# Optimization experiments

Measured on AMD Instinct MI355X. Metric: run time of the kernel, lower is better.

The kernel has to match this reference:

```python
import jax, jax.numpy as jnp
import numpy as np

B, S, D, V = 2, 4096, 2048, 32000
H, HD = 16, 128          # heads, head dim (H*HD == D)
BS = 16                  # block_size
N_ANCH = 128             # num_anchors (static: loss_mask=ones guarantees enough valid positions)
MASK_ID = 31999
DFF = 8192


def rms(x, w, eps=1e-6):
    return x * jax.lax.rsqrt(jnp.mean(x * x, axis=-1, keepdims=True) + eps) * w


def rope(x, pos):
    # x: (..., L, H, hd), pos: (..., L)
    hd = x.shape[-1]
    inv = 1.0 / (10000.0 ** (jnp.arange(0, hd, 2, dtype=jnp.float32) / hd))
    ang = pos[..., None, None].astype(jnp.float32) * inv  # (..., L, 1, hd/2)
    cos, sin = jnp.cos(ang), jnp.sin(ang)
    x1, x2 = x[..., : hd // 2], x[..., hd // 2 :]
    return jnp.concatenate([x1 * cos - x2 * sin, x2 * cos + x1 * sin], axis=-1).astype(x.dtype)


def setup_inputs() -> dict:
    key = jax.random.key(0)
    ks = jax.random.split(key, 12)
    s = 0.02
    return {
        "input_ids": jax.random.randint(ks[0], (B, S), 0, V, dtype=jnp.int32),
        "hidden_states": jax.random.normal(ks[1], (B, S, D), dtype=jnp.float32),
        "loss_mask": jnp.ones((B, S), dtype=jnp.float32),
        "rand_vals": jax.random.uniform(ks[2], (B, S - BS + 1), dtype=jnp.float32),
        "embed_table": jax.random.normal(ks[3], (V, D), dtype=jnp.float32) * s,
        "lm_head_w": jax.random.normal(ks[4], (V, D), dtype=jnp.float32) * s,
        "wq": jax.random.normal(ks[5], (D, D), dtype=jnp.float32) * s,
        "wk": jax.random.normal(ks[6], (D, D), dtype=jnp.float32) * s,
        "wv": jax.random.normal(ks[7], (D, D), dtype=jnp.float32) * s,
        "wo": jax.random.normal(ks[8], (D, D), dtype=jnp.float32) * s,
        "w_gate": jax.random.normal(ks[9], (D, DFF), dtype=jnp.float32) * s,
        "w_up": jax.random.normal(ks[10], (D, DFF), dtype=jnp.float32) * s,
        "w_down": jax.random.normal(ks[11], (DFF, D), dtype=jnp.float32) * s,
        "norm_attn": jnp.ones((D,), dtype=jnp.float32),
        "norm_mlp": jnp.ones((D,), dtype=jnp.float32),
        "norm_out": jnp.ones((D,), dtype=jnp.float32),
        "norm_chs": jnp.ones((D,), dtype=jnp.float32),
    }


def reference(input_ids, hidden_states, loss_mask, rand_vals, embed_table, lm_head_w,
              wq, wk, wv, wo, w_gate, w_up, w_down, norm_attn, norm_mlp, norm_out, norm_chs):
    max_anchor = S - BS
    # ---- anchor sampling: random permutation of valid positions via argsort of rand ----
    valid = loss_mask[:, : max_anchor + 1] > 0.5                       # (B, max_anchor+1)
    valid_counts = valid.sum(axis=1)
    idx = jnp.arange(max_anchor + 1, dtype=jnp.int32)
    masked_idx = jnp.where(valid, idx[None, :], S + 1)
    rv = jnp.where(valid, rand_vals, 2.0)
    order = jnp.argsort(rv, axis=1)
    gathered = jnp.take_along_axis(masked_idx, order, axis=1)
    anchors = jnp.sort(gathered[:, :N_ANCH], axis=1)                   # (B, N)
    keep = jnp.arange(N_ANCH)[None, :] < jnp.minimum(valid_counts, N_ANCH)[:, None]
    anchors = jnp.where(keep, anchors, 0)
    # ---- noise embedding: anchor token at block start, mask token elsewhere ----
    anchor_tok = jnp.take_along_axis(input_ids, jnp.clip(anchors, 0, S - 1), axis=1)
    first_tok = jnp.where(keep, anchor_tok, MASK_ID)
    noise_ids = jnp.full((B, N_ANCH, BS), MASK_ID, dtype=jnp.int32).at[:, :, 0].set(first_tok)
    x = embed_table[noise_ids]                                         # (B,N,BS,D)
    # ---- CHS context hidden: target hidden at anchor-1 ----
    ctx_pos = jnp.maximum(anchors - 1, 0)
    ctx = jnp.take_along_axis(hidden_states, ctx_pos[:, :, None], axis=1)  # (B,N,D)
    # ---- block-diagonal attention: per-block kv = [CHS_i | draft block i] (kv_len=1+BS) ----
    pos_q = anchors[:, :, None] + jnp.arange(BS)[None, None, :]        # (B,N,BS)
    pos_kv = jnp.concatenate([ctx_pos[:, :, None], pos_q], axis=2)     # (B,N,1+BS)
    hq = rms(x, norm_attn)
    hc = rms(ctx, norm_chs)[:, :, None, :]
    kv_in = jnp.concatenate([hc, hq], axis=2)                          # (B,N,1+BS,D)
    q = rope((hq @ wq).reshape(B, N_ANCH, BS, H, HD), pos_q)
    k = rope((kv_in @ wk).reshape(B, N_ANCH, 1 + BS, H, HD), pos_kv)
    v = (kv_in @ wv).reshape(B, N_ANCH, 1 + BS, H, HD)
    scores = jnp.einsum('bnqhd,bnkhd->bnhqk', q, k) * (1.0 / HD ** 0.5)
    attn = jax.nn.softmax(scores, axis=-1)
    out = jnp.einsum('bnhqk,bnkhd->bnqhd', attn, v).reshape(B, N_ANCH, BS, D) @ wo
    out = out * keep[:, :, None, None].astype(out.dtype)               # invalid blocks fully masked
    x = x + out
    h = rms(x, norm_mlp)
    x = x + (jax.nn.silu(h @ w_gate) * (h @ w_up)) @ w_down
    h_out = rms(x, norm_out)
    logits = h_out @ lm_head_w.T                                       # (B,N,BS,V)
    # ---- block-wise CE loss ----
    label_idx = anchors[:, :, None] + jnp.arange(BS)[None, None, :]
    valid_label = label_idx < S
    safe = jnp.minimum(label_idx, S - 1)
    targets = jnp.take_along_axis(jnp.broadcast_to(input_ids[:, None, :], (B, N_ANCH, S)), safe, axis=2)
    lm_g = jnp.take_along_axis(jnp.broadcast_to(loss_mask[:, None, :], (B, N_ANCH, S)), safe, axis=2)
    weight = (keep[:, :, None] & valid_label).astype(jnp.float32)
    weight = weight * (jnp.arange(BS) > 0)[None, None, :].astype(jnp.float32) * lm_g
    logp = jax.nn.log_softmax(logits, axis=-1)
    tok_logp = jnp.take_along_axis(logp, targets[..., None].astype(jnp.int32), axis=-1)[..., 0]
    loss = -(tok_logp * weight).sum() / (weight.sum() + 1e-6)
    pred = jnp.argmax(logits, axis=-1)
    accuracy = ((pred == targets) & (weight > 0.5)).sum().astype(jnp.float32) / (weight.sum() + 1e-6)
    return loss, accuracy
```

## Files before the change

### kernel.cpp

```cpp
#include <hip/hip_runtime.h>
#include <math.h>

typedef unsigned short u16;
typedef unsigned char u8;
typedef short v8s __attribute__((ext_vector_type(8)));
typedef u16   v4u __attribute__((ext_vector_type(4)));
typedef float v4f __attribute__((ext_vector_type(4)));
typedef int   v2i __attribute__((ext_vector_type(2)));

#define DEVFN static __device__ __forceinline__

constexpr int cB = 2, cS = 4096, cD = 2048, cV = 32000, cH = 16, cHD = 128;
constexpr int cBS = 16, cNA = 128, cMASK = 31999, cDFF = 8192;
constexpr int NCAND = cS - cBS + 1;
constexpr int MTOK  = cB * cNA * cBS;
constexpr int MKV   = cB * cNA * 17;
constexpr int NCH   = cV / 128;
constexpr int NCH2  = cV / 256;

constexpr int EPI_BF16 = 0, EPI_SILU = 1, EPI_OEMB = 2, EPI_DOWNACC = 3, EPI_STATS = 4;
constexpr int ASRC_BF16 = 0, ASRC_RMS = 1, ASRC_AOMAP = 2;

struct RmsSrc {
  const float* hs; const float* emb; const float* nattn; const float* nchs;
  const float* rowinv; const int* ftok; const int* cpos;
};

DEVFN u16 f2bf(float f) {
  union { float f; unsigned u; } a; a.f = f;
  unsigned u = a.u;
  u = u + 0x7fffu + ((u >> 16) & 1u);
  return (u16)(u >> 16);
}
DEVFN float bf2f(u16 h) {
  union { unsigned u; float f; } a; a.u = ((unsigned)h) << 16;
  return a.f;
}
DEVFN float waveSum(float v) {
  #pragma unroll
  for (int o = 32; o >= 1; o >>= 1) v += __shfl_xor(v, o);
  return v;
}
DEVFN void gload16(void* lds, const void* g) {
  __builtin_amdgcn_global_load_lds(
      (const __attribute__((address_space(1))) unsigned*)g,
      (__attribute__((address_space(3))) unsigned*)lds, 16, 0, 0);
}
DEVFN int pack4fp8(float a, float b, float c, float d) {
  int p = __builtin_amdgcn_cvt_pk_fp8_f32(a, b, 0, 0);
  p = __builtin_amdgcn_cvt_pk_fp8_f32(c, d, p, 1);
  return p;
}

__global__ void k_select(const float* __restrict__ lmask, const float* __restrict__ rv_in,
                         int* __restrict__ self) {
  int b = blockIdx.x >> 4, chunk = blockIdx.x & 15;
  __shared__ float rvs[4096];
  for (int i = threadIdx.x; i < NCAND; i += 256) {
    bool valid = lmask[(size_t)b * cS + i] > 0.5f;
    rvs[i] = valid ? rv_in[(size_t)b * NCAND + i] : 2.0f;
  }
  __syncthreads();
  int i = chunk * 256 + threadIdx.x;
  if (i < NCAND) {
    float v = rvs[i];
    int rank = 0;
    for (int j = 0; j < NCAND; ++j) {
      float u = rvs[j];
      rank += (u < v) || (u == v && j < i);
    }
    self[(size_t)b * NCAND + i] = (rank < cNA) ? 1 : 0;
  }
}

__global__ void k_anchors(const float* __restrict__ lmask, const int* __restrict__ self,
                          const int* __restrict__ ids, int* __restrict__ anchors,
                          int* __restrict__ keepA, int* __restrict__ ftok, int* __restrict__ cpos) {
  int b = blockIdx.x;
  __shared__ int flags[4096];
  __shared__ int ssum[256];
  __shared__ int soff[257];
  __shared__ int abuf[cNA];
  for (int i = threadIdx.x; i < 4096; i += 256)
    flags[i] = (i < NCAND) ? (self[(size_t)b * NCAND + i] && (lmask[(size_t)b * cS + i] > 0.5f)) : 0;
  if (threadIdx.x < cNA) abuf[threadIdx.x] = 0;
  __syncthreads();
  int s = 0;
  #pragma unroll
  for (int j = 0; j < 16; ++j) s += flags[threadIdx.x * 16 + j];
  ssum[threadIdx.x] = s;
  __syncthreads();
  if (threadIdx.x == 0) {
    int a = 0;
    for (int t = 0; t < 256; ++t) { soff[t] = a; a += ssum[t]; }
    soff[256] = a;
  }
  __syncthreads();
  int nsel = soff[256];
  int p = soff[threadIdx.x];
  for (int j = 0; j < 16; ++j) {
    int i = threadIdx.x * 16 + j;
    if (flags[i]) { if (p < cNA) abuf[p] = i; ++p; }
  }
  __syncthreads();
  if (threadIdx.x < cNA) {
    int q = threadIdx.x;
    int kp = (q < nsel) ? 1 : 0;
    int a = kp ? abuf[q] : 0;
    anchors[b * cNA + q] = a;
    keepA[b * cNA + q] = kp;
    int av = a; if (av < 0) av = 0; if (av > cS - 1) av = cS - 1;
    int tok = ids[(size_t)b * cS + av];
    ftok[b * cNA + q] = kp ? tok : cMASK;
    cpos[b * cNA + q] = (a - 1 > 0) ? (a - 1) : 0;
  }
}

__global__ void k_rowinv(const float* __restrict__ hs, const float* __restrict__ emb,
                         const int* __restrict__ ftok, const int* __restrict__ cpos,
                         float* __restrict__ rowinv) {
  int r = blockIdx.x;
  int j = r % 17, bn = r / 17, b = bn >> 7;
  const float* src = (j == 0) ? hs + ((size_t)b * cS + cpos[bn]) * cD
                              : emb + (size_t)((j == 1) ? ftok[bn] : cMASK) * cD;
  float ss = 0.f;
  for (int d = threadIdx.x; d < cD; d += 256) { float v = src[d]; ss += v * v; }
  ss = waveSum(ss);
  __shared__ float red[4];
  if ((threadIdx.x & 63) == 0) red[threadIdx.x >> 6] = ss;
  __syncthreads();
  if (threadIdx.x == 0) {
    float tot = red[0] + red[1] + red[2] + red[3];
    rowinv[r] = 1.0f / sqrtf(tot / cD + 1e-6f);
  }
}

__global__ void k_build2(const float* __restrict__ hs, const float* __restrict__ emb,
                         const float* __restrict__ nattn, const float* __restrict__ nchs,
                         const int* __restrict__ ftok, const int* __restrict__ cpos,
                         u16* __restrict__ kv) {
  int r = blockIdx.x;
  int j = r % 17, bn = r / 17, b = bn >> 7;
  const float* src; const float* w;
  if (j == 0) { src = hs + ((size_t)b * cS + cpos[bn]) * cD; w = nchs; }
  else {
    int tok = (j == 1) ? ftok[bn] : cMASK;
    src = emb + (size_t)tok * cD; w = nattn;
  }
  float ss = 0.f;
  for (int d = threadIdx.x; d < cD; d += 256) { float v = src[d]; ss += v * v; }
  ss = waveSum(ss);
  __shared__ float red[4];
  if ((threadIdx.x & 63) == 0) red[threadIdx.x >> 6] = ss;
  __syncthreads();
  float tot = red[0] + red[1] + red[2] + red[3];
  float inv = 1.0f / sqrtf(tot / cD + 1e-6f);
  for (int d = threadIdx.x; d < cD; d += 256)
    kv[(size_t)r * cD + d] = f2bf(src[d] * inv * w[d]);
}

__global__ void k_rms(const float* __restrict__ xin, const float* __restrict__ w,
                      u16* __restrict__ outp) {
  int m = blockIdx.x;
  const float* row = xin + (size_t)m * cD;
  float ss = 0.f;
  for (int d = threadIdx.x; d < cD; d += 256) { float v = row[d]; ss += v * v; }
  ss = waveSum(ss);
  __shared__ float red[4];
  if ((threadIdx.x & 63) == 0) red[threadIdx.x >> 6] = ss;
  __syncthreads();
  float tot = red[0] + red[1] + red[2] + red[3];
  float inv = 1.0f / sqrtf(tot / cD + 1e-6f);
  for (int d = threadIdx.x; d < cD; d += 256)
    outp[(size_t)m * cD + d] = f2bf(row[d] * inv * w[d]);
}

__global__ void k_conv8(const float* __restrict__ in, u8* __restrict__ out, long n, float scale) {
  long i = ((long)blockIdx.x * 256 + threadIdx.x) * 8;
  long stride = (long)gridDim.x * 256 * 8;
  for (; i < n; i += stride) {
    v4f a = *(const v4f*)(in + i), b = *(const v4f*)(in + i + 4);
    v2i pk;
    pk[0] = pack4fp8(a[0] * scale, a[1] * scale, a[2] * scale, a[3] * scale);
    pk[1] = pack4fp8(b[0] * scale, b[1] * scale, b[2] * scale, b[3] * scale);
    *(v2i*)(out + i) = pk;
  }
}

__global__ void k_cvt8(const u16* __restrict__ in, u8* __restrict__ out, long n) {
  long i = ((long)blockIdx.x * 256 + threadIdx.x) * 8;
  long stride = (long)gridDim.x * 256 * 8;
  for (; i < n; i += stride) {
    v8s a = *(const v8s*)(in + i);
    v2i pk;
    pk[0] = pack4fp8(bf2f((u16)a[0]), bf2f((u16)a[1]), bf2f((u16)a[2]), bf2f((u16)a[3]));
    pk[1] = pack4fp8(bf2f((u16)a[4]), bf2f((u16)a[5]), bf2f((u16)a[6]), bf2f((u16)a[7]));
    *(v2i*)(out + i) = pk;
  }
}

__global__ void k_tconv(const float* __restrict__ W, u16* __restrict__ WT, int K, int N) {
  __shared__ u16 t[64][72];
  int n0 = blockIdx.x * 64, k0 = blockIdx.y * 64;
  int tid = threadIdx.x;
  int c4 = (tid & 15) * 4, r0 = tid >> 4;
  #pragma unroll
  for (int rr = 0; rr < 64; rr += 16) {
    int k = r0 + rr;
    v4f v = *(const v4f*)(W + (size_t)(k0 + k) * N + n0 + c4);
    #pragma unroll
    for (int e = 0; e < 4; ++e) t[c4 + e][k] = f2bf(v[e]);
  }
  __syncthreads();
  int n = tid >> 2, kq = (tid & 3) * 16;
  v8s o0, o1;
  #pragma unroll
  for (int e = 0; e < 8; ++e) { o0[e] = (short)t[n][kq + e]; o1[e] = (short)t[n][kq + 8 + e]; }
  *(v8s*)(WT + (size_t)(n0 + n) * K + k0 + kq) = o0;
  *(v8s*)(WT + (size_t)(n0 + n) * K + k0 + kq + 8) = o1;
}

template <int EPI>
__launch_bounds__(512, 1)
__global__ void k_gemm6(const u16* __restrict__ Abf, const u16* __restrict__ Bbf,
                        u16* __restrict__ Cbf, const u16* __restrict__ Gaux,
                        v4f* __restrict__ partials, int K, int ldc, int nch) {
  __shared__ __align__(16) u16 lds[65536];
  const int tid = threadIdx.x;
  const int lane = tid & 63, wid = tid >> 6;
  const int wm = wid >> 2, wn = wid & 3;
  const int lc = lane & 15, lq = lane >> 4;
  const int m0 = blockIdx.x * 256, n0 = blockIdx.y * 256;

  const u16* srcA[2]; const u16* srcB[2];
  #pragma unroll
  for (int i = 0; i < 2; ++i) {
    int s = i * 512 + tid;
    int row = s >> 2;
    int c2 = (s & 3) ^ ((row >> 1) & 3);
    srcA[i] = Abf + (size_t)(m0 + row) * K + c2 * 8;
    srcB[i] = Bbf + (size_t)(n0 + row) * K + c2 * 8;
  }

  v4f acc[8][4];
  #pragma unroll
  for (int i = 0; i < 8; ++i)
    #pragma unroll
    for (int j = 0; j < 4; ++j) acc[i][j] = (v4f){0.f, 0.f, 0.f, 0.f};

  const int fsw = lq ^ ((lc >> 1) & 3);
  int aoff[8], boff[4];
  #pragma unroll
  for (int mi = 0; mi < 8; ++mi) aoff[mi] = ((wm * 128 + mi * 16 + lc) * 4 + fsw) * 8;
  #pragma unroll
  for (int ni = 0; ni < 4; ++ni) boff[ni] = ((wn * 64 + ni * 16 + lc) * 4 + fsw) * 8;

  auto stageA = [&](int t, int kh) {
    int reg = (t & 1) * 32768 + kh * 8192;
    int koff = t * 64 + kh * 32;
    #pragma unroll
    for (int i = 0; i < 2; ++i)
      gload16(&lds[reg + i * 4096 + wid * 512], srcA[i] + koff);
  };
  auto stageB = [&](int t, int kh) {
    int reg = (t & 1) * 32768 + 16384 + kh * 8192;
    int koff = t * 64 + kh * 32;
    #pragma unroll
    for (int i = 0; i < 2; ++i)
      gload16(&lds[reg + i * 4096 + wid * 512], srcB[i] + koff);
  };

  stageA(0, 0); stageB(0, 0);
  stageA(0, 1); stageB(0, 1);
  stageA(1, 0); stageB(1, 0);
  asm volatile("s_waitcnt vmcnt(8)" ::: "memory");
  __builtin_amdgcn_s_barrier();

  const int NT = K >> 6;
  for (int t = 0; t < NT; ++t) {
    const int bufb = (t & 1) * 32768;
    const u16* Ab0 = &lds[bufb];
    const u16* Ab1 = &lds[bufb + 8192];
    const u16* Bb0 = &lds[bufb + 16384];
    const u16* Bb1 = &lds[bufb + 24576];
    v8s a_[4], b_[4];

    #pragma unroll
    for (int ni = 0; ni < 4; ++ni) b_[ni] = *(const v8s*)(Bb0 + boff[ni]);
    #pragma unroll
    for (int mi = 0; mi < 4; ++mi) a_[mi] = *(const v8s*)(Ab0 + aoff[mi]);
    if (t + 1 < NT) stageA(t + 1, 1);
    asm volatile("s_waitcnt lgkmcnt(0)" ::: "memory");
    __builtin_amdgcn_sched_barrier(0);
    __builtin_amdgcn_s_setprio(1);
    #pragma unroll
    for (int mi = 0; mi < 4; ++mi)
      #pragma unroll
      for (int ni = 0; ni < 4; ++ni)
        acc[mi][ni] = __builtin_amdgcn_mfma_f32_16x16x32_bf16(a_[mi], b_[ni], acc[mi][ni], 0, 0, 0);
    __builtin_amdgcn_s_setprio(0);
    __builtin_amdgcn_s_barrier();

    #pragma unroll
    for (int mi = 0; mi < 4; ++mi) a_[mi] = *(const v8s*)(Ab0 + aoff[mi + 4]);
    if (t + 1 < NT) stageB(t + 1, 1);
    asm volatile("s_waitcnt lgkmcnt(0)" ::: "memory");
    __builtin_amdgcn_sched_barrier(0);
    __builtin_amdgcn_s_setprio(1);
    #pragma unroll
    for (int mi = 0; mi < 4; ++mi)
      #pragma unroll
      for (int ni = 0; ni < 4; ++ni)
        acc[mi + 4][ni] = __builtin_amdgcn_mfma_f32_16x16x32_bf16(a_[mi], b_[ni], acc[mi + 4][ni], 0, 0, 0);
    __builtin_amdgcn_s_setprio(0);
    if (t + 1 < NT) { asm volatile("s_waitcnt vmcnt(4)" ::: "memory"); }
    else            { asm volatile("s_waitcnt vmcnt(0)" ::: "memory"); }
    __builtin_amdgcn_s_barrier();

    #pragma unroll
    for (int ni = 0; ni < 4; ++ni) b_[ni] = *(const v8s*)(Bb1 + boff[ni]);
    #pragma unroll
    for (int mi = 0; mi < 4; ++mi) a_[mi] = *(const v8s*)(Ab1 + aoff[mi]);
    if (t + 2 < NT) stageA(t + 2, 0);
    asm volatile("s_waitcnt lgkmcnt(0)" ::: "memory");
    __builtin_amdgcn_sched_barrier(0);
    __builtin_amdgcn_s_setprio(1);
    #pragma unroll
    for (int mi = 0; mi < 4; ++mi)
      #pragma unroll
      for (int ni = 0; ni < 4; ++ni)
        acc[mi][ni] = __builtin_amdgcn_mfma_f32_16x16x32_bf16(a_[mi], b_[ni], acc[mi][ni], 0, 0, 0);
    __builtin_amdgcn_s_setprio(0);
    __builtin_amdgcn_s_barrier();

    #pragma unroll
    for (int mi = 0; mi < 4; ++mi) a_[mi] = *(const v8s*)(Ab1 + aoff[mi + 4]);
    if (t + 2 < NT) stageB(t + 2, 0);
    asm volatile("s_waitcnt lgkmcnt(0)" ::: "memory");
    __builtin_amdgcn_sched_barrier(0);
    __builtin_amdgcn_s_setprio(1);
    #pragma unroll
    for (int mi = 0; mi < 4; ++mi)
      #pragma unroll
      for (int ni = 0; ni < 4; ++ni)
        acc[mi + 4][ni] = __builtin_amdgcn_mfma_f32_16x16x32_bf16(a_[mi], b_[ni], acc[mi + 4][ni], 0, 0, 0);
    __builtin_amdgcn_s_setprio(0);
    __builtin_amdgcn_s_barrier();
  }
  asm volatile("s_waitcnt vmcnt(0)" ::: "memory");

  #pragma unroll
  for (int mi = 0; mi < 8; ++mi)
    #pragma unroll
    for (int ni = 0; ni < 4; ++ni)
      #pragma unroll
      for (int r = 0; r < 4; ++r) {
        int grow = m0 + wm * 128 + mi * 16 + lq * 4 + r;
        int gcol = n0 + wn * 64 + ni * 16 + lc;
        size_t idx = (size_t)grow * ldc + gcol;
        float vv = acc[mi][ni][r];
        if constexpr (EPI == EPI_BF16) {
          Cbf[idx] = f2bf(vv);
        } else {
          float g = bf2f(Gaux[idx]);
          Cbf[idx] = f2bf(vv * g / (1.0f + __expf(-g)));
        }
      }
  (void)partials; (void)nch;
}

__launch_bounds__(512, 2)
__global__ void k_gemm7(const u8* __restrict__ A8, const u8* __restrict__ B8,
                        v4f* __restrict__ partials, int K, int nch) {
  __shared__ __align__(16) u8 lds8[65536];
  const int tid = threadIdx.x;
  const int lane = tid & 63, wid = tid >> 6;
  const int wm = wid >> 2, wn = wid & 3;
  const int lc = lane & 15, lq = lane >> 4;
  const int m0 = blockIdx.x * 256, n0 = blockIdx.y * 256;

  const u8* srcA; const u8* srcB;
  {
    int row = tid >> 1;
    int cl = (tid & 1) ^ ((row >> 2) & 1);
    srcA = A8 + (size_t)(m0 + row) * K + cl * 16;
    srcB = B8 + (size_t)(n0 + row) * K + cl * 16;
  }

  v4f acc[8][4];
  #pragma unroll
  for (int i = 0; i < 8; ++i)
    #pragma unroll
    for (int j = 0; j < 4; ++j) acc[i][j] = (v4f){0.f, 0.f, 0.f, 0.f};

  int aoff[8], boff[4];
  #pragma unroll
  for (int mi = 0; mi < 8; ++mi) {
    int row = wm * 128 + mi * 16 + lc;
    aoff[mi] = row * 32 + (lq ^ (((row >> 2) & 1) << 1)) * 8;
  }
  #pragma unroll
  for (int ni = 0; ni < 4; ++ni) {
    int row = wn * 64 + ni * 16 + lc;
    boff[ni] = row * 32 + (lq ^ (((row >> 2) & 1) << 1)) * 8;
  }

  auto stageA = [&](int t, int kh) {
    int reg = (t & 1) * 32768 + kh * 8192;
    gload16(&lds8[reg + wid * 1024], srcA + t * 64 + kh * 32);
  };
  auto stageB = [&](int t, int kh) {
    int reg = (t & 1) * 32768 + 16384 + kh * 8192;
    gload16(&lds8[reg + wid * 1024], srcB + t * 64 + kh * 32);
  };

  stageA(0, 0); stageB(0, 0);
  stageA(0, 1); stageB(0, 1);
  stageA(1, 0); stageB(1, 0);
  asm volatile("s_waitcnt vmcnt(4)" ::: "memory");
  __builtin_amdgcn_s_barrier();

  const int NT = K >> 6;
  for (int t = 0; t < NT; ++t) {
    const int bufb = (t & 1) * 32768;
    const u8* Ab0 = &lds8[bufb];
    const u8* Ab1 = &lds8[bufb + 8192];
    const u8* Bb0 = &lds8[bufb + 16384];
    const u8* Bb1 = &lds8[bufb + 24576];
    long long a_[4], b_[4];

    #pragma unroll
    for (int ni = 0; ni < 4; ++ni) b_[ni] = *(const long long*)(Bb0 + boff[ni]);
    #pragma unroll
    for (int mi = 0; mi < 4; ++mi) a_[mi] = *(const long long*)(Ab0 + aoff[mi]);
    if (t + 1 < NT) stageA(t + 1, 1);
    asm volatile("s_waitcnt lgkmcnt(0)" ::: "memory");
    __builtin_amdgcn_sched_barrier(0);
    __builtin_amdgcn_s_setprio(1);
    #pragma unroll
    for (int mi = 0; mi < 4; ++mi)
      #pragma unroll
      for (int ni = 0; ni < 4; ++ni)
        acc[mi][ni] = __builtin_amdgcn_mfma_f32_16x16x32_fp8_fp8(a_[mi], b_[ni], acc[mi][ni], 0, 0, 0);
    __builtin_amdgcn_s_setprio(0);
    __builtin_amdgcn_s_barrier();

    #pragma unroll
    for (int mi = 0; mi < 4; ++mi) a_[mi] = *(const long long*)(Ab0 + aoff[mi + 4]);
    if (t + 1 < NT) stageB(t + 1, 1);
    asm volatile("s_waitcnt lgkmcnt(0)" ::: "memory");
    __builtin_amdgcn_sched_barrier(0);
    __builtin_amdgcn_s_setprio(1);
    #pragma unroll
    for (int mi = 0; mi < 4; ++mi)
      #pragma unroll
      for (int ni = 0; ni < 4; ++ni)
        acc[mi + 4][ni] = __builtin_amdgcn_mfma_f32_16x16x32_fp8_fp8(a_[mi], b_[ni], acc[mi + 4][ni], 0, 0, 0);
    __builtin_amdgcn_s_setprio(0);
    if (t + 1 < NT) { asm volatile("s_waitcnt vmcnt(4)" ::: "memory"); }
    else            { asm volatile("s_waitcnt vmcnt(0)" ::: "memory"); }
    __builtin_amdgcn_s_barrier();

    #pragma unroll
    for (int ni = 0; ni < 4; ++ni) b_[ni] = *(const long long*)(Bb1 + boff[ni]);
    #pragma unroll
    for (int mi = 0; mi < 4; ++mi) a_[mi] = *(const long long*)(Ab1 + aoff[mi]);
    if (t + 2 < NT) stageA(t + 2, 0);
    asm volatile("s_waitcnt lgkmcnt(0)" ::: "memory");
    __builtin_amdgcn_sched_barrier(0);
    __builtin_amdgcn_s_setprio(1);
    #pragma unroll
    for (int mi = 0; mi < 4; ++mi)
      #pragma unroll
      for (int ni = 0; ni < 4; ++ni)
        acc[mi][ni] = __builtin_amdgcn_mfma_f32_16x16x32_fp8_fp8(a_[mi], b_[ni], acc[mi][ni], 0, 0, 0);
    __builtin_amdgcn_s_setprio(0);
    __builtin_amdgcn_s_barrier();

    #pragma unroll
    for (int mi = 0; mi < 4; ++mi) a_[mi] = *(const long long*)(Ab1 + aoff[mi + 4]);
    if (t + 2 < NT) stageB(t + 2, 0);
    asm volatile("s_waitcnt lgkmcnt(0)" ::: "memory");
    __builtin_amdgcn_sched_barrier(0);
    __builtin_amdgcn_s_setprio(1);
    #pragma unroll
    for (int mi = 0; mi < 4; ++mi)
      #pragma unroll
      for (int ni = 0; ni < 4; ++ni)
        acc[mi + 4][ni] = __builtin_amdgcn_mfma_f32_16x16x32_fp8_fp8(a_[mi], b_[ni], acc[mi + 4][ni], 0, 0, 0);
    __builtin_amdgcn_s_setprio(0);
    __builtin_amdgcn_s_barrier();
  }
  asm volatile("s_waitcnt vmcnt(0)" ::: "memory");

  #pragma unroll
  for (int mi = 0; mi < 8; ++mi)
    #pragma unroll
    for (int ni = 0; ni < 4; ++ni)
      acc[mi][ni] *= 0.015625f;

  __shared__ float s_mx[1024], s_sm[1024];
  __shared__ int   s_ax[1024];
  __syncthreads();
  #pragma unroll
  for (int mi = 0; mi < 8; ++mi) {
    #pragma unroll
    for (int r = 0; r < 4; ++r) {
      float v0 = acc[mi][0][r], v1 = acc[mi][1][r], v2 = acc[mi][2][r], v3 = acc[mi][3][r];
      float mx = v0; int ax = lc;
      if (v1 > mx) { mx = v1; ax = 16 + lc; }
      if (v2 > mx) { mx = v2; ax = 32 + lc; }
      if (v3 > mx) { mx = v3; ax = 48 + lc; }
      #pragma unroll
      for (int off = 1; off < 16; off <<= 1) {
        float om = __shfl_xor(mx, off); int oa = __shfl_xor(ax, off);
        if (om > mx || (om == mx && oa < ax)) { mx = om; ax = oa; }
      }
      float se = __expf(v0 - mx) + __expf(v1 - mx) + __expf(v2 - mx) + __expf(v3 - mx);
      #pragma unroll
      for (int off = 1; off < 16; off <<= 1) se += __shfl_xor(se, off);
      if (lc == 0) {
        int row = wm * 128 + mi * 16 + lq * 4 + r;
        s_mx[row * 4 + wn] = mx; s_sm[row * 4 + wn] = se; s_ax[row * 4 + wn] = wn * 64 + ax;
      }
    }
  }
  __syncthreads();
  if (tid < 256) {
    float gm = s_mx[tid * 4]; int ga = s_ax[tid * 4];
    #pragma unroll
    for (int w = 1; w < 4; ++w) {
      float m = s_mx[tid * 4 + w];
      if (m > gm) { gm = m; ga = s_ax[tid * 4 + w]; }
    }
    float gs = 0.f;
    #pragma unroll
    for (int w = 0; w < 4; ++w) gs += s_sm[tid * 4 + w] * __expf(s_mx[tid * 4 + w] - gm);
    v4f rec; rec[0] = gm; rec[1] = gs; rec[2] = __int_as_float(n0 + ga); rec[3] = 0.f;
    partials[(size_t)(m0 + tid) * nch + blockIdx.y] = rec;
  }
}

template <int ASRC, int EPI>
__launch_bounds__(256, 2)
__global__ void k_gemm4(const u16* __restrict__ Abf, const u16* __restrict__ Bbf,
                        u16* __restrict__ Cbf, float* __restrict__ Cf32,
                        const int* __restrict__ keepArr, RmsSrc rs, int K, int ldb, int ldc) {
  __shared__ __align__(16) u16 lds[2][16384];
  const int tid = threadIdx.x;
  const int lane = tid & 63, wid = tid >> 6;
  const int wm = wid >> 1, wn = wid & 1;
  const int lc = lane & 15, lq = lane >> 4;
  const int m0 = blockIdx.x * 128, n0 = blockIdx.y * 128;

  const u16* srcA[4]; const u16* srcB[4];
  #pragma unroll
  for (int i = 0; i < 4; ++i) {
    int s = i * 256 + tid;
    int row = s >> 3;
    int c3 = (s & 7) ^ (row & 7);
    int ar = m0 + row;
    if constexpr (ASRC == ASRC_AOMAP) ar = (ar >> 4) * 17 + 1 + (ar & 15);
    srcA[i] = Abf + (size_t)ar * K + c3 * 8;
    srcB[i] = Bbf + (size_t)(n0 + row) * ldb + c3 * 8;
  }

  v4f acc[4][4];
  #pragma unroll
  for (int i = 0; i < 4; ++i)
    #pragma unroll
    for (int j = 0; j < 4; ++j) acc[i][j] = (v4f){0.f, 0.f, 0.f, 0.f};

  const int sw = lc & 7;
  const int aoff0 = (((wm * 64 + lc) * 8 + 0 + lq) ^ sw) * 8;
  const int aoff1 = (((wm * 64 + lc) * 8 + 4 + lq) ^ sw) * 8;
  const int boff0 = (((wn * 64 + lc) * 8 + 0 + lq) ^ sw) * 8;
  const int boff1 = (((wn * 64 + lc) * 8 + 4 + lq) ^ sw) * 8;

  auto stageTo = [&](int b) {
    u16* dA = &lds[b][0] + wid * 512;
    u16* dB = &lds[b][8192] + wid * 512;
    #pragma unroll
    for (int i = 0; i < 4; ++i) { gload16(dA + i * 2048, srcA[i]); srcA[i] += 64; }
    #pragma unroll
    for (int i = 0; i < 4; ++i) { gload16(dB + i * 2048, srcB[i]); srcB[i] += 64; }
  };

  stageTo(0);
  const int NT = K >> 6;
  for (int t = 0; t < NT; ++t) {
    const int cur = t & 1;
    if (t + 1 < NT) {
      stageTo(cur ^ 1);
      asm volatile("s_waitcnt vmcnt(8)" ::: "memory");
    } else {
      asm volatile("s_waitcnt vmcnt(0)" ::: "memory");
    }
    __builtin_amdgcn_s_barrier();
    const u16* Ab = &lds[cur][0];
    const u16* Bb = &lds[cur][8192];
    v8s a0[4], a1[4], b0[4], b1[4];
    #pragma unroll
    for (int mi = 0; mi < 4; ++mi) a0[mi] = *(const v8s*)(Ab + aoff0 + mi * 1024);
    #pragma unroll
    for (int ni = 0; ni < 4; ++ni) b0[ni] = *(const v8s*)(Bb + boff0 + ni * 1024);
    #pragma unroll
    for (int mi = 0; mi < 4; ++mi) a1[mi] = *(const v8s*)(Ab + aoff1 + mi * 1024);
    #pragma unroll
    for (int ni = 0; ni < 4; ++ni) b1[ni] = *(const v8s*)(Bb + boff1 + ni * 1024);
    __builtin_amdgcn_s_setprio(1);
    #pragma unroll
    for (int mi = 0; mi < 4; ++mi)
      #pragma unroll
      for (int ni = 0; ni < 4; ++ni)
        acc[mi][ni] = __builtin_amdgcn_mfma_f32_16x16x32_bf16(a0[mi], b0[ni], acc[mi][ni], 0, 0, 0);
    __builtin_amdgcn_s_setprio(0);
    asm volatile("s_waitcnt lgkmcnt(0)" ::: "memory");
    __builtin_amdgcn_sched_barrier(0);
    __builtin_amdgcn_s_barrier();
    __builtin_amdgcn_s_setprio(1);
    #pragma unroll
    for (int mi = 0; mi < 4; ++mi)
      #pragma unroll
      for (int ni = 0; ni < 4; ++ni)
        acc[mi][ni] = __builtin_amdgcn_mfma_f32_16x16x32_bf16(a1[mi], b1[ni], acc[mi][ni], 0, 0, 0);
    __builtin_amdgcn_s_setprio(0);
  }

  #pragma unroll
  for (int mi = 0; mi < 4; ++mi)
    #pragma unroll
    for (int ni = 0; ni < 4; ++ni)
      #pragma unroll
      for (int r = 0; r < 4; ++r) {
        int grow = m0 + wm * 64 + mi * 16 + lq * 4 + r;
        int gcol = n0 + wn * 64 + ni * 16 + lc;
        size_t idx = (size_t)grow * ldc + gcol;
        float vv = acc[mi][ni][r];
        if constexpr (EPI == EPI_BF16) {
          Cbf[idx] = f2bf(vv);
        } else if constexpr (EPI == EPI_OEMB) {
          int t_ = grow & 15, bn = grow >> 4;
          int tok = (t_ == 0) ? rs.ftok[bn] : cMASK;
          float kf = (float)keepArr[bn];
          Cf32[idx] = rs.emb[(size_t)tok * cD + gcol] + vv * kf;
        } else {
          Cf32[idx] += vv;
        }
      }
}

template <int ASRC, int BLAYOUT, int EPI>
__launch_bounds__(256)
__global__ void k_gemm(const u16* __restrict__ Abf, const float* __restrict__ Bw,
                       u16* Cbf, float* Cf32, const u16* Gaux,
// ... 269 lines not shown
__global__ void k_final(const float* __restrict__ tokOut, float* __restrict__ outp) {
  int tid = threadIdx.x;
  float swl = 0.f, sw = 0.f, sm = 0.f;
  for (int m = tid; m < MTOK; m += 256) {
    swl += tokOut[m * 4 + 0];
    sw  += tokOut[m * 4 + 1];
    sm  += tokOut[m * 4 + 2];
  }
  swl = waveSum(swl); sw = waveSum(sw); sm = waveSum(sm);
  __shared__ float r0[4], r1[4], r2[4];
  int lane = tid & 63, w = tid >> 6;
  if (lane == 0) { r0[w] = swl; r1[w] = sw; r2[w] = sm; }
  __syncthreads();
  if (tid == 0) {
    float a = r0[0] + r0[1] + r0[2] + r0[3];
    float b = r1[0] + r1[1] + r1[2] + r1[3];
    float c = r2[0] + r2[1] + r2[2] + r2[3];
    float denom = b + 1e-6f;
    float loss = -a / denom;
    float acc  = c / denom;
    if (b == 0.0f) loss = -300.0f;
    outp[0] = loss;
    outp[1] = acc;
  }
}

__global__ void k_heartbeat(float* outp) {
  if (threadIdx.x == 0) { outp[0] = -55.0f; outp[1] = -55.0f; }
}
__global__ void k_sentinel(float* outp) {
  if (threadIdx.x == 0) { outp[0] = -777.0f; outp[1] = -777.0f; }
}

extern "C" void kernel_launch(void* const* d_in, const int* in_sizes, int n_in,
                              void* d_out, int out_size, void* d_ws, size_t ws_size,
                              hipStream_t stream) {
  const int*   ids   = (const int*)  d_in[0];
  const float* hs    = (const float*)d_in[1];
  const float* lmask = (const float*)d_in[2];
  const float* rv    = (const float*)d_in[3];
  const float* emb   = (const float*)d_in[4];
  const float* wlm   = (const float*)d_in[5];
  const float* wq    = (const float*)d_in[6];
  const float* wk    = (const float*)d_in[7];
  const float* wv    = (const float*)d_in[8];
  const float* wo    = (const float*)d_in[9];
  const float* wg    = (const float*)d_in[10];
  const float* wu    = (const float*)d_in[11];
  const float* wd    = (const float*)d_in[12];
  const float* nattn = (const float*)d_in[13];
  const float* nmlp  = (const float*)d_in[14];
  const float* nout  = (const float*)d_in[15];
  const float* nchs  = (const float*)d_in[16];
  (void)in_sizes; (void)n_in; (void)out_size;

  float* outp = (float*)d_out;
  k_heartbeat<<<dim3(1), 64, 0, stream>>>(outp);

  char* wsb = (char*)d_ws;
  size_t off = 0;
  auto alloc = [&](size_t bytes) -> void* {
    void* p = wsb + off;
    off = (off + bytes + 255) & ~(size_t)255;
    return p;
  };
  int*   anchors = (int*)  alloc((size_t)cB * cNA * 4);
  int*   keepA   = (int*)  alloc((size_t)cB * cNA * 4);
  int*   ftok    = (int*)  alloc((size_t)cB * cNA * 4);
  int*   cpos    = (int*)  alloc((size_t)cB * cNA * 4);
  int*   self    = (int*)  alloc((size_t)cB * NCAND * 4);
  float* rowinv  = (float*)alloc((size_t)MKV * 4);
  int*   ttok    = (int*)  alloc((size_t)MTOK * 4);
  float* tlogit  = (float*)alloc((size_t)MTOK * 4);
  float* tokOut  = (float*)alloc((size_t)MTOK * 4 * 4);

  const size_t szQ  = (size_t)MKV * cD * 2;
  const size_t szX  = (size_t)MTOK * cD * 4;
  u16* qb = (u16*)alloc(szQ);
  const size_t a1off = off;

  RmsSrc rs{hs, emb, nattn, nchs, rowinv, ftok, cpos};

  k_select <<<dim3(cB * 16), 256, 0, stream>>>(lmask, rv, self);
  k_anchors<<<dim3(cB),      256, 0, stream>>>(lmask, self, ids, anchors, keepA, ftok, cpos);

  const size_t szKV   = szQ;
  const size_t szCbuf = (size_t)MTOK * 4096 * 2;
  size_t kvb_off  = a1off;
  size_t a1f_off  = (kvb_off + szKV + 255) & ~(size_t)255;
  size_t a1f_sz   = 2 * szQ > (szX + szCbuf) ? 2 * szQ : (szX + szCbuf);
  size_t wreg_off = (a1f_off + a1f_sz + 255) & ~(size_t)255;
  size_t wreg_sz  = (size_t)cV * cD * 2;
  size_t need_fast = wreg_off + wreg_sz;

  if (need_fast <= ws_size) {
    u16*   kvb   = (u16*)(wsb + kvb_off);
    u16*   kb    = (u16*)(wsb + a1f_off);
    u16*   vb    = (u16*)(wsb + a1f_off + szQ);
    float* xb    = (float*)(wsb + a1f_off);
    u16*   cbuf  = (u16*)(wsb + a1f_off + szX);
    v4f*   parts = (v4f*)(wsb + a1f_off);
    u8*    h8    = (u8*)(wsb + a1f_off + (size_t)16 * 1024 * 1024);
    u16*   hb    = qb;
    u16*   houtb = qb;
    u16*   wT    = (u16*)(wsb + wreg_off);
    const size_t szDD = (size_t)cD * cD;
    u16* wqT = wT;            u16* wkT = wT + szDD;
    u16* wvT = wT + 2 * szDD; u16* woT = wT + 3 * szDD;
    const size_t szDF = (size_t)cD * cDFF;
    u16* wgT = wT; u16* wuT = wT + szDF; u16* wdT = wT + 2 * szDF;
    u8*  wlm8 = (u8*)wT;

    k_build2<<<dim3(MKV), 256, 0, stream>>>(hs, emb, nattn, nchs, ftok, cpos, kvb);

    k_tconv<<<dim3(32, 32), 256, 0, stream>>>(wq, wqT, cD, cD);
    k_tconv<<<dim3(32, 32), 256, 0, stream>>>(wk, wkT, cD, cD);
    k_tconv<<<dim3(32, 32), 256, 0, stream>>>(wv, wvT, cD, cD);
    k_tconv<<<dim3(32, 32), 256, 0, stream>>>(wo, woT, cD, cD);

    k_gemm4<ASRC_BF16, EPI_BF16><<<dim3(MKV / 128, cD / 128), 256, 0, stream>>>(
        kvb, wqT, qb, nullptr, nullptr, rs, cD, cD, cD);
    k_gemm4<ASRC_BF16, EPI_BF16><<<dim3(MKV / 128, cD / 128), 256, 0, stream>>>(
        kvb, wkT, kb, nullptr, nullptr, rs, cD, cD, cD);
    k_gemm4<ASRC_BF16, EPI_BF16><<<dim3(MKV / 128, cD / 128), 256, 0, stream>>>(
        kvb, wvT, vb, nullptr, nullptr, rs, cD, cD, cD);

    k_rope<<<dim3(2 * MKV), 256, 0, stream>>>(qb, kb, anchors, cpos);
    k_attn<<<dim3(cB * cNA * cH), 64, 0, stream>>>(qb, kb, vb);

    k_gemm4<ASRC_AOMAP, EPI_OEMB><<<dim3(MTOK / 128, cD / 128), 256, 0, stream>>>(
        qb, woT, nullptr, xb, keepA, rs, cD, cD, cD);

    k_rms<<<dim3(MTOK), 256, 0, stream>>>(xb, nmlp, hb);

    k_tconv<<<dim3(128, 32), 256, 0, stream>>>(wg, wgT, cD, cDFF);
    k_tconv<<<dim3(128, 32), 256, 0, stream>>>(wu, wuT, cD, cDFF);
    k_tconv<<<dim3(32, 128), 256, 0, stream>>>(wd, wdT, cDFF, cD);

    for (int cb = 0; cb < cDFF; cb += 4096) {
      k_gemm6<EPI_BF16><<<dim3(MTOK / 256, 16), 512, 0, stream>>>(
          hb, wgT + (size_t)cb * cD, cbuf, nullptr, nullptr, cD, 4096, 0);
      k_gemm6<EPI_SILU><<<dim3(MTOK / 256, 16), 512, 0, stream>>>(
          hb, wuT + (size_t)cb * cD, cbuf, cbuf, nullptr, cD, 4096, 0);
      k_gemm4<ASRC_BF16, EPI_DOWNACC><<<dim3(MTOK / 128, cD / 128), 256, 0, stream>>>(
          cbuf, wdT + cb, nullptr, xb, nullptr, rs, 4096, cDFF, cD);
    }

    k_rms<<<dim3(MTOK), 256, 0, stream>>>(xb, nout, houtb);

    k_tgt<<<dim3(MTOK / 4), 256, 0, stream>>>(houtb, wlm, ids, anchors, ttok, tlogit);

    k_cvt8 <<<dim3(1024), 256, 0, stream>>>(houtb, h8, (long)MTOK * cD);
    k_conv8<<<dim3(2048), 256, 0, stream>>>(wlm, wlm8, (long)cV * cD, 64.0f);
    k_gemm7<<<dim3(MTOK / 256, NCH2), 512, 0, stream>>>(h8, wlm8, parts, cD, NCH2);

    k_combine<<<dim3(MTOK), 256, 0, stream>>>(parts, ttok, tlogit, keepA, anchors, lmask, tokOut, NCH2);
    k_final  <<<dim3(1), 256, 0, stream>>>(tokOut, outp);
    return;
  }

  const int cwopts[4] = {4096, 2048, 1024, 512};
  int CW = 0;
  for (int ci = 0; ci < 4; ++ci) {
    int cw = cwopts[ci];
    size_t cbufsz = (size_t)MTOK * cw * 2;
    size_t s1 = 2 * szQ;
    size_t s2 = szX + cbufsz;
    size_t sz = s1 > s2 ? s1 : s2;
    size_t pmin = (size_t)MTOK * NCH * 16;
    if (pmin > sz) sz = pmin;
    if (a1off + sz <= ws_size) { CW = cw; break; }
  }
  if (CW == 0) { k_sentinel<<<dim3(1), 64, 0, stream>>>(outp); return; }

  u16*   kb    = (u16*)(wsb + a1off);
  u16*   vb    = (u16*)(wsb + a1off + szQ);
  float* xb    = (float*)(wsb + a1off);
  u16*   cbuf  = (u16*)(wsb + a1off + szX);
  v4f*   parts = (v4f*)(wsb + a1off);
  u16*   hb    = qb;
  u16*   houtb = qb;

  k_rowinv<<<dim3(MKV), 256, 0, stream>>>(hs, emb, ftok, cpos, rowinv);

  k_gemm<ASRC_RMS, 0, EPI_BF16><<<dim3(MKV / 128, cD / 128), 256, 0, stream>>>(
      nullptr, wq, qb, nullptr, nullptr, nullptr, nullptr, rs, cD, cD, cD);
  k_gemm<ASRC_RMS, 0, EPI_BF16><<<dim3(MKV / 128, cD / 128), 256, 0, stream>>>(
      nullptr, wk, kb, nullptr, nullptr, nullptr, nullptr, rs, cD, cD, cD);
  k_gemm<ASRC_RMS, 0, EPI_BF16><<<dim3(MKV / 128, cD / 128), 256, 0, stream>>>(
      nullptr, wv, vb, nullptr, nullptr, nullptr, nullptr, rs, cD, cD, cD);

  k_rope<<<dim3(2 * MKV), 256, 0, stream>>>(qb, kb, anchors, cpos);
  k_attn<<<dim3(cB * cNA * cH), 64, 0, stream>>>(qb, kb, vb);

  k_gemm<ASRC_AOMAP, 0, EPI_OEMB><<<dim3(MTOK / 128, cD / 128), 256, 0, stream>>>(
      qb, wo, nullptr, xb, nullptr, keepA, nullptr, rs, cD, cD, cD);

  k_rms<<<dim3(MTOK), 256, 0, stream>>>(xb, nmlp, hb);

  for (int cb = 0; cb < cDFF; cb += CW) {
    k_gemm<ASRC_BF16, 0, EPI_BF16><<<dim3(MTOK / 128, CW / 128), 256, 0, stream>>>(
        hb, wg + cb, cbuf, nullptr, nullptr, nullptr, nullptr, rs, cD, cDFF, CW);
    k_gemm<ASRC_BF16, 0, EPI_SILU><<<dim3(MTOK / 128, CW / 128), 256, 0, stream>>>(
        hb, wu + cb, cbuf, nullptr, cbuf, nullptr, nullptr, rs, cD, cDFF, CW);
    k_gemm<ASRC_BF16, 0, EPI_DOWNACC><<<dim3(MTOK / 128, cD / 128), 256, 0, stream>>>(
        cbuf, wd + (size_t)cb * cD, nullptr, xb, nullptr, nullptr, nullptr, rs, CW, cD, cD);
  }

  k_rms<<<dim3(MTOK), 256, 0, stream>>>(xb, nout, houtb);

  k_tgt<<<dim3(MTOK / 4), 256, 0, stream>>>(houtb, wlm, ids, anchors, ttok, tlogit);
  k_gemm<ASRC_BF16, 1, EPI_STATS><<<dim3(MTOK / 128, cV / 128), 256, 0, stream>>>(
      houtb, wlm, nullptr, nullptr, nullptr, nullptr, parts, rs, cD, cD, 0);

  k_combine<<<dim3(MTOK), 256, 0, stream>>>(parts, ttok, tlogit, keepA, anchors, lmask, tokOut, NCH);
  k_final  <<<dim3(1), 256, 0, stream>>>(tokOut, outp);
}
```

Measured before the change: 1.614 ms.

## Permute fp8 operand layout so GEMM fetches 16-byte fragments covering two K-steps

```diff
diff --git a/kernel.cpp b/kernel.cpp
--- a/kernel.cpp
+++ b/kernel.cpp
@@ -7,6 +7,7 @@
 typedef u16   v4u __attribute__((ext_vector_type(4)));
 typedef float v4f __attribute__((ext_vector_type(4)));
 typedef int   v2i __attribute__((ext_vector_type(2)));
+typedef int   v4i __attribute__((ext_vector_type(4)));
 
 #define DEVFN static __device__ __forceinline__
 
@@ -50,6 +51,9 @@
   int p = __builtin_amdgcn_cvt_pk_fp8_f32(a, b, 0, 0);
   p = __builtin_amdgcn_cvt_pk_fp8_f32(c, d, p, 1);
   return p;
+}
+DEVFN long perm8(long i) {
+  return (i & ~63L) | (((i >> 3) & 3) << 4) | (((i >> 5) & 1) << 3);
 }
 
 __global__ void k_select(const float* __restrict__ lmask, const float* __restrict__ rv_in,
@@ -183,7 +187,7 @@
     v2i pk;
     pk[0] = pack4fp8(a[0] * scale, a[1] * scale, a[2] * scale, a[3] * scale);
     pk[1] = pack4fp8(b[0] * scale, b[1] * scale, b[2] * scale, b[3] * scale);
-    *(v2i*)(out + i) = pk;
+    *(v2i*)(out + perm8(i)) = pk;
   }
 }
 
@@ -195,7 +199,7 @@
     v2i pk;
     pk[0] = pack4fp8(bf2f((u16)a[0]), bf2f((u16)a[1]), bf2f((u16)a[2]), bf2f((u16)a[3]));
     pk[1] = pack4fp8(bf2f((u16)a[4]), bf2f((u16)a[5]), bf2f((u16)a[6]), bf2f((u16)a[7]));
-    *(v2i*)(out + i) = pk;
+    *(v2i*)(out + perm8(i)) = pk;
   }
 }
 
@@ -370,7 +374,7 @@
 }
 
 __launch_bounds__(512, 2)
-__global__ void k_gemm7(const u8* __restrict__ A8, const u8* __restrict__ B8,
+__global__ void k_gemm8(const u8* __restrict__ A8, const u8* __restrict__ B8,
                         v4f* __restrict__ partials, int K, int nch) {
   __shared__ __align__(16) u8 lds8[65536];
   const int tid = threadIdx.x;
@@ -379,12 +383,14 @@
   const int lc = lane & 15, lq = lane >> 4;
   const int m0 = blockIdx.x * 256, n0 = blockIdx.y * 256;
 
-  const u8* srcA; const u8* srcB;
-  {
-    int row = tid >> 1;
-    int cl = (tid & 1) ^ ((row >> 2) & 1);
-    srcA = A8 + (size_t)(m0 + row) * K + cl * 16;
-    srcB = B8 + (size_t)(n0 + row) * K + cl * 16;
+  const u8* srcA[2]; const u8* srcB[2];
+  #pragma unroll
+  for (int i = 0; i < 2; ++i) {
+    int ci = i * 512 + tid;
+    int r = ci >> 2;
+    int logc = (ci & 3) ^ ((r >> 1) & 3);
+    srcA[i] = A8 + (size_t)(m0 + r) * K + logc * 16;
+    srcB[i] = B8 + (size_t)(n0 + r) * K + logc * 16;
   }
 
   v4f acc[8][4];
@@ -393,47 +399,36 @@
     #pragma unroll
     for (int j = 0; j < 4; ++j) acc[i][j] = (v4f){0.f, 0.f, 0.f, 0.f};
 
+  const int csw = (lc >> 1) & 3;
   int aoff[8], boff[4];
   #pragma unroll
-  for (int mi = 0; mi < 8; ++mi) {
-    int row = wm * 128 + mi * 16 + lc;
-    aoff[mi] = row * 32 + (lq ^ (((row >> 2) & 1) << 1)) * 8;
-  }
-  #pragma unroll
-  for (int ni = 0; ni < 4; ++ni) {
-    int row = wn * 64 + ni * 16 + lc;
-    boff[ni] = row * 32 + (lq ^ (((row >> 2) & 1) << 1)) * 8;
-  }
-
-  auto stageA = [&](int t, int kh) {
-    int reg = (t & 1) * 32768 + kh * 8192;
-    gload16(&lds8[reg + wid * 1024], srcA + t * 64 + kh * 32);
+  for (int mi = 0; mi < 8; ++mi) aoff[mi] = (wm * 128 + mi * 16 + lc) * 64 + ((lq ^ csw) << 4);
+  #pragma unroll
+  for (int ni = 0; ni < 4; ++ni) boff[ni] = (wn * 64 + ni * 16 + lc) * 64 + ((lq ^ csw) << 4);
+
+  auto stageA = [&](int t, int i) {
+    gload16(&lds8[(t & 1) * 32768 + i * 8192 + wid * 1024], srcA[i] + t * 64);
   };
-  auto stageB = [&](int t, int kh) {
-    int reg = (t & 1) * 32768 + 16384 + kh * 8192;
-    gload16(&lds8[reg + wid * 1024], srcB + t * 64 + kh * 32);
+  auto stageB = [&](int t, int i) {
+    gload16(&lds8[(t & 1) * 32768 + 16384 + i * 8192 + wid * 1024], srcB[i] + t * 64);
   };
 
-  stageA(0, 0); stageB(0, 0);
-  stageA(0, 1); stageB(0, 1);
-  stageA(1, 0); stageB(1, 0);
+  stageA(0, 0); stageA(0, 1); stageB(0, 0); stageB(0, 1);
+  stageA(1, 0); stageA(1, 1); stageB(1, 0); stageB(1, 1);
   asm volatile("s_waitcnt vmcnt(4)" ::: "memory");
   __builtin_amdgcn_s_barrier();
 
+  union Frag { v4i v; long long ll[2]; };
   const int NT = K >> 6;
   for (int t = 0; t < NT; ++t) {
-    const int bufb = (t & 1) * 32768;
-    const u8* Ab0 = &lds8[bufb];
-    const u8* Ab1 = &lds8[bufb + 8192];
-    const u8* Bb0 = &lds8[bufb + 16384];
-    const u8* Bb1 = &lds8[bufb + 24576];
-    long long a_[4], b_[4];
-
-    #pragma unroll
-    for (int ni = 0; ni < 4; ++ni) b_[ni] = *(const long long*)(Bb0 + boff[ni]);
-    #pragma unroll
-    for (int mi = 0; mi < 4; ++mi) a_[mi] = *(const long long*)(Ab0 + aoff[mi]);
-    if (t + 1 < NT) stageA(t + 1, 1);
+    const u8* Ab = &lds8[(t & 1) * 32768];
+    const u8* Bb = Ab + 16384;
+    Frag fa[8], fb[4];
+
+    #pragma unroll
+    for (int ni = 0; ni < 4; ++ni) fb[ni].v = *(const v4i*)(Bb + boff[ni]);
+    #pragma unroll
+    for (int mi = 0; mi < 4; ++mi) fa[mi].v = *(const v4i*)(Ab + aoff[mi]);
     asm volatile("s_waitcnt lgkmcnt(0)" ::: "memory");
     __builtin_amdgcn_sched_barrier(0);
     __builtin_amdgcn_s_setprio(1);
@@ -441,44 +436,12 @@
     for (int mi = 0; mi < 4; ++mi)
       #pragma unroll
       for (int ni = 0; ni < 4; ++ni)
-        acc[mi][ni] = __builtin_amdgcn_mfma_f32_16x16x32_fp8_fp8(a_[mi], b_[ni], acc[mi][ni], 0, 0, 0);
+        acc[mi][ni] = __builtin_amdgcn_mfma_f32_16x16x32_fp8_fp8(fa[mi].ll[0], fb[ni].ll[0], acc[mi][ni], 0, 0, 0);
     __builtin_amdgcn_s_setprio(0);
     __builtin_amdgcn_s_barrier();
 
     #pragma unroll
-    for (int mi = 0; mi < 4; ++mi) a_[mi] = *(const long long*)(Ab0 + aoff[mi + 4]);
-    if (t + 1 < NT) stageB(t + 1, 1);
-    asm volatile("s_waitcnt lgkmcnt(0)" ::: "memory");
-    __builtin_amdgcn_sched_barrier(0);
-    __builtin_amdgcn_s_setprio(1);
-    #pragma unroll
-    for (int mi = 0; mi < 4; ++mi)
-      #pragma unroll
-      for (int ni = 0; ni < 4; ++ni)
-        acc[mi + 4][ni] = __builtin_amdgcn_mfma_f32_16x16x32_fp8_fp8(a_[mi], b_[ni], acc[mi + 4][ni], 0, 0, 0);
-    __builtin_amdgcn_s_setprio(0);
-    if (t + 1 < NT) { asm volatile("s_waitcnt vmcnt(4)" ::: "memory"); }
-    else            { asm volatile("s_waitcnt vmcnt(0)" ::: "memory"); }
-    __builtin_amdgcn_s_barrier();
-
-    #pragma unroll
-    for (int ni = 0; ni < 4; ++ni) b_[ni] = *(const long long*)(Bb1 + boff[ni]);
-    #pragma unroll
-    for (int mi = 0; mi < 4; ++mi) a_[mi] = *(const long long*)(Ab1 + aoff[mi]);
-    if (t + 2 < NT) stageA(t + 2, 0);
-    asm volatile("s_waitcnt lgkmcnt(0)" ::: "memory");
-    __builtin_amdgcn_sched_barrier(0);
-    __builtin_amdgcn_s_setprio(1);
-    #pragma unroll
-    for (int mi = 0; mi < 4; ++mi)
-      #pragma unroll
-      for (int ni = 0; ni < 4; ++ni)
-        acc[mi][ni] = __builtin_amdgcn_mfma_f32_16x16x32_fp8_fp8(a_[mi], b_[ni], acc[mi][ni], 0, 0, 0);
-    __builtin_amdgcn_s_setprio(0);
-    __builtin_amdgcn_s_barrier();
-
-    #pragma unroll
-    for (int mi = 0; mi < 4; ++mi) a_[mi] = *(const long long*)(Ab1 + aoff[mi + 4]);
+    for (int mi = 0; mi < 4; ++mi) fa[mi + 4].v = *(const v4i*)(Ab + aoff[mi + 4]);
     if (t + 2 < NT) stageB(t + 2, 0);
     asm volatile("s_waitcnt lgkmcnt(0)" ::: "memory");
     __builtin_amdgcn_sched_barrier(0);
@@ -487,9 +450,31 @@
     for (int mi = 0; mi < 4; ++mi)
       #pragma unroll
       for (int ni = 0; ni < 4; ++ni)
-        acc[mi + 4][ni] = __builtin_amdgcn_mfma_f32_16x16x32_fp8_fp8(a_[mi], b_[ni], acc[mi + 4][ni], 0, 0, 0);
+        acc[mi + 4][ni] = __builtin_amdgcn_mfma_f32_16x16x32_fp8_fp8(fa[mi + 4].ll[0], fb[ni].ll[0], acc[mi + 4][ni], 0, 0, 0);
     __builtin_amdgcn_s_setprio(0);
     __builtin_amdgcn_s_barrier();
+
+    if (t + 2 < NT) { stageB(t + 2, 1); stageA(t + 2, 0); }
+    __builtin_amdgcn_s_setprio(1);
+    #pragma unroll
+    for (int mi = 0; mi < 4; ++mi)
+      #pragma unroll
+      for (int ni = 0; ni < 4; ++ni)
+        acc[mi][ni] = __builtin_amdgcn_mfma_f32_16x16x32_fp8_fp8(fa[mi].ll[1], fb[ni].ll[1], acc[mi][ni], 0, 0, 0);
+    __builtin_amdgcn_s_setprio(0);
+    __builtin_amdgcn_s_barrier();
+
+    if (t + 2 < NT) stageA(t + 2, 1);
+    __builtin_amdgcn_s_setprio(1);
+    #pragma unroll
+    for (int mi = 0; mi < 4; ++mi)
+      #pragma unroll
+      for (int ni = 0; ni < 4; ++ni)
+        acc[mi + 4][ni] = __builtin_amdgcn_mfma_f32_16x16x32_fp8_fp8(fa[mi + 4].ll[1], fb[ni].ll[1], acc[mi + 4][ni], 0, 0, 0);
+    __builtin_amdgcn_s_setprio(0);
+    if (t + 2 < NT) { asm volatile("s_waitcnt vmcnt(4)" ::: "memory"); }
+    else            { asm volatile("s_waitcnt vmcnt(0)" ::: "memory"); }
+    __builtin_amdgcn_s_barrier();
   }
   asm volatile("s_waitcnt vmcnt(0)" ::: "memory");
 
@@ -499,8 +484,9 @@
     for (int ni = 0; ni < 4; ++ni)
       acc[mi][ni] *= 0.015625f;
 
-  __shared__ float s_mx[1024], s_sm[1024];
-  __shared__ int   s_ax[1024];
+  float* s_mx = (float*)lds8;
+  float* s_sm = (float*)(lds8 + 4096);
+  int*   s_ax = (int*)(lds8 + 8192);
   __syncthreads();
   #pragma unroll
   for (int mi = 0; mi < 8; ++mi) {
@@ -1076,7 +1062,7 @@
 
     k_cvt8 <<<dim3(1024), 256, 0, stream>>>(houtb, h8, (long)MTOK * cD);
     k_conv8<<<dim3(2048), 256, 0, stream>>>(wlm, wlm8, (long)cV * cD, 64.0f);
-    k_gemm7<<<dim3(MTOK / 256, NCH2), 512, 0, stream>>>(h8, wlm8, parts, cD, NCH2);
+    k_gemm8<<<dim3(MTOK / 256, NCH2), 512, 0, stream>>>(h8, wlm8, parts, cD, NCH2);
 
     k_combine<<<dim3(MTOK), 256, 0, stream>>>(parts, ttok, tlogit, keepA, anchors, lmask, tokOut, NCH2);
     k_final  <<<dim3(1), 256, 0, stream>>>(tokOut, outp);
```

After: 1.557 ms. 3.6% less time.
